# Performance work log

Hardware: AMD Instinct MI355X
Metric: run time of the kernel (lower is better)

The kernel has to match this reference:

```python
import jax, jax.numpy as jnp
import numpy as np

B, K, C, O, I = 32, 1024, 64, 32, 32  # batch, num_capsules, num_classes, out_dim, in_dim
NUM_ROUTING = 3


def squash(x, axis=-1):
    sq = jnp.sum(x * x, axis=axis, keepdims=True)
    return (sq / (1.0 + sq)) * x / jnp.sqrt(sq + 1e-8)


def setup_inputs() -> dict:
    key = jax.random.key(0)
    kx, kw = jax.random.split(key)
    x = jax.random.normal(kx, (B, K, I), dtype=jnp.float32)
    W = jax.random.normal(kw, (K, C, O, I), dtype=jnp.float32) * 0.01
    return {"x": x, "W": W}


def reference(x, W):
    # u_hat[b,k,c,o] = sum_i W[k,c,o,i] * x[b,k,i]  (the torch repeat+matmul)
    u_hat = jnp.einsum('kcoi,bki->bkco', W, x)  # [B,K,C,O]
    b_ij = jnp.zeros((B, K, C, 1), dtype=x.dtype)
    c_ij = None
    v_j = None
    for i in range(NUM_ROUTING):
        c_ij = jax.nn.softmax(b_ij, axis=2)              # softmax over classes
        s_j = jnp.sum(c_ij * u_hat, axis=1, keepdims=True)  # [B,1,C,O]
        v_j = squash(s_j, axis=-1)
        if i < NUM_ROUTING - 1:
            agreement = jnp.sum(u_hat * v_j, axis=-1, keepdims=True)  # [B,K,C,1]
            b_ij = b_ij + agreement
    return v_j[:, 0], c_ij[..., 0]  # ([B,C,O], [B,K,C])
```

## Files before the change

kernel.cpp:

```cpp
#include <hip/hip_runtime.h>
#include <stdint.h>

#define Bb 32
#define Kk 1024
#define Cc 64
#define Oo 32
#define Ii 32

typedef __attribute__((ext_vector_type(8))) short bf16x8;
typedef __attribute__((ext_vector_type(4))) float f32x4;

__device__ __forceinline__ short f2bf(float f) {
    uint32_t u = __builtin_bit_cast(uint32_t, f);
    u += 0x7fffu + ((u >> 16) & 1u);
    return (short)(u >> 16);
}
__device__ __forceinline__ float bflo(uint32_t u) { return __builtin_bit_cast(float, u << 16); }
__device__ __forceinline__ float bfhi(uint32_t u) { return __builtin_bit_cast(float, u & 0xffff0000u); }
__device__ __forceinline__ uint32_t pk2(float a, float b) {
    return (uint32_t)(uint16_t)f2bf(a) | ((uint32_t)(uint16_t)f2bf(b) << 16);
}


__global__ __launch_bounds__(256) void k_uhat(const float* __restrict__ x,
                                              const float* __restrict__ W,
                                              uint32_t* __restrict__ uh) {
    const int k = blockIdx.x;
    const int lane = threadIdx.x & 63;
    const int wave = threadIdx.x >> 6;
    const int m = lane & 15;
    const int q = lane >> 4;

    bf16x8 bfrag[2];
#pragma unroll
    for (int nb = 0; nb < 2; ++nb) {
        const float* xp = x + (size_t)((nb * 16 + m) * Kk + k) * Ii + q * 8;
        f32x4 a = *(const f32x4*)xp;
        f32x4 b = *(const f32x4*)(xp + 4);
        bf16x8 t;
        t[0] = f2bf(a.x); t[1] = f2bf(a.y); t[2] = f2bf(a.z); t[3] = f2bf(a.w);
        t[4] = f2bf(b.x); t[5] = f2bf(b.y); t[6] = f2bf(b.z); t[7] = f2bf(b.w);
        bfrag[nb] = t;
    }

    for (int cc = 0; cc < 16; ++cc) {
        const int c = wave * 16 + cc;
        bf16x8 afrag[2];
#pragma unroll
        for (int mo = 0; mo < 2; ++mo) {
            const float* wp = W + (size_t)((k * Cc + c) * Oo + mo * 16 + m) * Ii + q * 8;
            f32x4 a = __builtin_nontemporal_load((const f32x4*)wp);
            f32x4 b = __builtin_nontemporal_load((const f32x4*)(wp + 4));
            bf16x8 t;
            t[0] = f2bf(a.x); t[1] = f2bf(a.y); t[2] = f2bf(a.z); t[3] = f2bf(a.w);
            t[4] = f2bf(b.x); t[5] = f2bf(b.y); t[6] = f2bf(b.z); t[7] = f2bf(b.w);
            afrag[mo] = t;
        }
        const f32x4 z = {0.f, 0.f, 0.f, 0.f};
        f32x4 d0 = __builtin_amdgcn_mfma_f32_16x16x32_bf16(afrag[0], bfrag[0], z, 0, 0, 0);
        f32x4 d1 = __builtin_amdgcn_mfma_f32_16x16x32_bf16(afrag[0], bfrag[1], z, 0, 0, 0);
        f32x4 d2 = __builtin_amdgcn_mfma_f32_16x16x32_bf16(afrag[1], bfrag[0], z, 0, 0, 0);
        f32x4 d3 = __builtin_amdgcn_mfma_f32_16x16x32_bf16(afrag[1], bfrag[1], z, 0, 0, 0);

        uint4 p0, p1;
        p0.x = pk2(d0.x, d0.y); p0.y = pk2(d0.z, d0.w);
        p0.z = pk2(d1.x, d1.y); p0.w = pk2(d1.z, d1.w);
        p1.x = pk2(d2.x, d2.y); p1.y = pk2(d2.z, d2.w);
        p1.z = pk2(d3.x, d3.y); p1.w = pk2(d3.z, d3.w);
        uint32_t* dst = uh + (size_t)(k * Cc + c) * 512 + lane * 4;
        *(uint4*)dst = p0;
        *(uint4*)(dst + 256) = p1;
    }
}

__global__ __launch_bounds__(256) void k_sacc0(const uint32_t* __restrict__ uh,
                                               float* __restrict__ part0) {
    const int lane = threadIdx.x & 63;
    const int wave = threadIdx.x >> 6;
    const int c = (blockIdx.x & 15) * 4 + wave;
    const int chunk = blockIdx.x >> 4;
    const int k0 = chunk * 32;

    float acc[16];
#pragma unroll
    for (int i = 0; i < 16; ++i) acc[i] = 0.f;

    for (int kl = 0; kl < 32; ++kl) {
        const uint32_t* up = uh + (size_t)((k0 + kl) * Cc + c) * 512 + lane * 4;
        uint4 q0 = *(const uint4*)up;
        uint4 q1 = *(const uint4*)(up + 256);
        const float w0 = 1.0f / 64.0f;
        acc[0]  += w0 * bflo(q0.x);  acc[1]  += w0 * bfhi(q0.x);
        acc[2]  += w0 * bflo(q0.y);  acc[3]  += w0 * bfhi(q0.y);
        acc[4]  += w0 * bflo(q0.z);  acc[5]  += w0 * bfhi(q0.z);
        acc[6]  += w0 * bflo(q0.w);  acc[7]  += w0 * bfhi(q0.w);
        acc[8]  += w0 * bflo(q1.x);  acc[9]  += w0 * bfhi(q1.x);
        acc[10] += w0 * bflo(q1.y);  acc[11] += w0 * bfhi(q1.y);
        acc[12] += w0 * bflo(q1.z);  acc[13] += w0 * bfhi(q1.z);
        acc[14] += w0 * bflo(q1.w);  acc[15] += w0 * bfhi(q1.w);
    }
#pragma unroll
    for (int t = 0; t < 4; ++t) {
        f32x4 v = {acc[t * 4 + 0], acc[t * 4 + 1], acc[t * 4 + 2], acc[t * 4 + 3]};
        *(f32x4*)&part0[(((size_t)(chunk * Cc + c) * 4 + t) * 64 + lane) * 4] = v;
    }
}

__global__ __launch_bounds__(256) void k_reduce0(const float* __restrict__ part0,
                                                 float* __restrict__ vfrag) {
    __shared__ float red[4 * 64 * 17];
    const int c = blockIdx.x;
    const int tid = threadIdx.x;
    const int lane = tid & 63;
    const int cg = tid >> 6;

    float acc[16];
#pragma unroll
    for (int i = 0; i < 16; ++i) acc[i] = 0.f;
    for (int ch = cg * 8; ch < cg * 8 + 8; ++ch) {
        const f32x4* p = (const f32x4*)part0 + (size_t)(ch * Cc + c) * 4 * 64 + lane;
#pragma unroll
        for (int t = 0; t < 4; ++t) {
            f32x4 v = p[t * 64];
            acc[t * 4 + 0] += v.x; acc[t * 4 + 1] += v.y;
            acc[t * 4 + 2] += v.z; acc[t * 4 + 3] += v.w;
        }
    }
#pragma unroll
    for (int i = 0; i < 16; ++i) red[(cg * 64 + lane) * 17 + i] = acc[i];
    __syncthreads();

    if (tid < 64) {
        float a[16];
#pragma unroll
        for (int i = 0; i < 16; ++i)
            a[i] = red[tid * 17 + i] + red[(64 + tid) * 17 + i]
                 + red[(128 + tid) * 17 + i] + red[(192 + tid) * 17 + i];
        float sq0 = 0.f, sq1 = 0.f;
#pragma unroll
        for (int r = 0; r < 4; ++r) {
            sq0 += a[r] * a[r] + a[8 + r] * a[8 + r];
            sq1 += a[4 + r] * a[4 + r] + a[12 + r] * a[12 + r];
        }
        sq0 += __shfl_xor(sq0, 16); sq0 += __shfl_xor(sq0, 32);
        sq1 += __shfl_xor(sq1, 16); sq1 += __shfl_xor(sq1, 32);
        const float c0 = sq0 / ((1.f + sq0) * sqrtf(sq0 + 1e-8f));
        const float c1 = sq1 / ((1.f + sq1) * sqrtf(sq1 + 1e-8f));
#pragma unroll
        for (int r = 0; r < 4; ++r) {
            a[r] *= c0; a[8 + r] *= c0;
            a[4 + r] *= c1; a[12 + r] *= c1;
        }
        float* vp = vfrag + ((size_t)c * 64 + tid) * 16;
#pragma unroll
        for (int t = 0; t < 4; ++t) {
            f32x4 v = {a[t * 4 + 0], a[t * 4 + 1], a[t * 4 + 2], a[t * 4 + 3]};
            *(f32x4*)(vp + t * 4) = v;
        }
    }
}

template <bool FINAL>
__global__ __launch_bounds__(512) void k_iter(const uint32_t* __restrict__ uh,
                                              const float* __restrict__ vfrag,
                                              float* __restrict__ bbuf,
                                              uint32_t* __restrict__ partB,
                                              float* __restrict__ outc) {
    __shared__ float agr[4 * 64 * 32];
    const int tid = threadIdx.x;
    const int lane = tid & 63;
    const int w = tid >> 6;
    const int m = lane & 15;
    const int q = lane >> 4;
    const int k0 = blockIdx.x * 4;

    for (int cc = 0; cc < 8; ++cc) {
        const int c = w * 8 + cc;
        const float* vp = vfrag + ((size_t)c * 64 + lane) * 16;
        f32x4 vv0 = *(const f32x4*)(vp);
        f32x4 vv1 = *(const f32x4*)(vp + 4);
        f32x4 vv2 = *(const f32x4*)(vp + 8);
        f32x4 vv3 = *(const f32x4*)(vp + 12);
#pragma unroll
        for (int kl = 0; kl < 4; ++kl) {
            const uint32_t* up = uh + (size_t)((k0 + kl) * Cc + c) * 512 + lane * 4;
            uint4 q0 = *(const uint4*)up;
            uint4 q1 = *(const uint4*)(up + 256);
            float p0 = bflo(q0.x) * vv0.x + bfhi(q0.x) * vv0.y
                     + bflo(q0.y) * vv0.z + bfhi(q0.y) * vv0.w
                     + bflo(q1.x) * vv2.x + bfhi(q1.x) * vv2.y
                     + bflo(q1.y) * vv2.z + bfhi(q1.y) * vv2.w;
            float p1 = bflo(q0.z) * vv1.x + bfhi(q0.z) * vv1.y
                     + bflo(q0.w) * vv1.z + bfhi(q0.w) * vv1.w
                     + bflo(q1.z) * vv3.x + bfhi(q1.z) * vv3.y
                     + bflo(q1.w) * vv3.z + bfhi(q1.w) * vv3.w;
            p0 += __shfl_xor(p0, 16);
            p0 += __shfl_xor(p0, 32);
            p1 += __shfl_xor(p1, 16);
            p1 += __shfl_xor(p1, 32);
            if (q == 0) {
                agr[(kl * 64 + c) * 32 + m] = p0;
                agr[(kl * 64 + c) * 32 + 16 + m] = p1;
            }
        }
    }
    __syncthreads();

    if (tid < 128) {
        const int kl = tid >> 5;
        const int b = tid & 31;
        const int k = k0 + kl;
        float row[64];
#pragma unroll
        for (int c = 0; c < 64; ++c) row[c] = agr[(kl * 64 + c) * 32 + b];
        if (!FINAL) {
            float* bp = bbuf + (size_t)(k * Bb + b) * Cc;
#pragma unroll
            for (int c = 0; c < 64; ++c) bp[c] = row[c];
        } else {
            const float* bp = bbuf + (size_t)(k * Bb + b) * Cc;
#pragma unroll
            for (int c = 0; c < 64; ++c) row[c] += bp[c];
        }
        float mx = row[0];
#pragma unroll
        for (int c = 1; c < 64; ++c) mx = fmaxf(mx, row[c]);
        float sum = 0.f;
#pragma unroll
        for (int c = 0; c < 64; ++c) { row[c] = __expf(row[c] - mx); sum += row[c]; }
        const float inv = 1.f / sum;
#pragma unroll
        for (int c = 0; c < 64; ++c) row[c] *= inv;
        if (FINAL) {
            float* op = outc + (size_t)(b * Kk + k) * Cc;
#pragma unroll
            for (int c = 0; c < 64; ++c) op[c] = row[c];
        }
#pragma unroll
        for (int c = 0; c < 64; ++c) agr[(kl * 64 + c) * 32 + b] = row[c];
    }
    __syncthreads();

    const int chunk = blockIdx.x;
    for (int cg = 0; cg < 8; ++cg) {
        const int c = w * 8 + cg;
        float acc[16];
#pragma unroll
        for (int i = 0; i < 16; ++i) acc[i] = 0.f;
#pragma unroll
        for (int kl = 0; kl < 4; ++kl) {
            const uint32_t* up = uh + (size_t)((k0 + kl) * Cc + c) * 512 + lane * 4;
            uint4 q0 = *(const uint4*)up;
            uint4 q1 = *(const uint4*)(up + 256);
            const float w0 = agr[(kl * 64 + c) * 32 + m];
            const float w1 = agr[(kl * 64 + c) * 32 + 16 + m];
            acc[0]  += w0 * bflo(q0.x);  acc[1]  += w0 * bfhi(q0.x);
            acc[2]  += w0 * bflo(q0.y);  acc[3]  += w0 * bfhi(q0.y);
            acc[4]  += w1 * bflo(q0.z);  acc[5]  += w1 * bfhi(q0.z);
            acc[6]  += w1 * bflo(q0.w);  acc[7]  += w1 * bfhi(q0.w);
            acc[8]  += w0 * bflo(q1.x);  acc[9]  += w0 * bfhi(q1.x);
            acc[10] += w0 * bflo(q1.y);  acc[11] += w0 * bfhi(q1.y);
            acc[12] += w1 * bflo(q1.z);  acc[13] += w1 * bfhi(q1.z);
            acc[14] += w1 * bflo(q1.w);  acc[15] += w1 * bfhi(q1.w);
        }
        uint4 o0, o1;
        o0.x = pk2(acc[0],  acc[1]);  o0.y = pk2(acc[2],  acc[3]);
        o0.z = pk2(acc[4],  acc[5]);  o0.w = pk2(acc[6],  acc[7]);
        o1.x = pk2(acc[8],  acc[9]);  o1.y = pk2(acc[10], acc[11]);
        o1.z = pk2(acc[12], acc[13]); o1.w = pk2(acc[14], acc[15]);
        uint32_t* dst = partB + ((size_t)(c * 256 + chunk) * 64 + lane) * 8;
        *(uint4*)dst = o0;
        *(uint4*)(dst + 4) = o1;
    }
}

__global__ __launch_bounds__(256) void k_red1(const uint32_t* __restrict__ partB,
                                              float* __restrict__ part2) {
    __shared__ float red[4 * 64 * 17];
    const int cb = blockIdx.x;
    const int c = cb >> 3;
    const int g = cb & 7;
    const int tid = threadIdx.x;
    const int lane = tid & 63;
    const int ww = tid >> 6;

    float acc[16];
#pragma unroll
    for (int i = 0; i < 16; ++i) acc[i] = 0.f;
    for (int ch = g * 32 + ww * 8; ch < g * 32 + ww * 8 + 8; ++ch) {
        const uint32_t* p = partB + ((size_t)(c * 256 + ch) * 64 + lane) * 8;
        uint4 a = *(const uint4*)p;
        uint4 b = *(const uint4*)(p + 4);
        acc[0]  += bflo(a.x);  acc[1]  += bfhi(a.x);
        acc[2]  += bflo(a.y);  acc[3]  += bfhi(a.y);
        acc[4]  += bflo(a.z);  acc[5]  += bfhi(a.z);
        acc[6]  += bflo(a.w);  acc[7]  += bfhi(a.w);
        acc[8]  += bflo(b.x);  acc[9]  += bfhi(b.x);
        acc[10] += bflo(b.y);  acc[11] += bfhi(b.y);
        acc[12] += bflo(b.z);  acc[13] += bfhi(b.z);
        acc[14] += bflo(b.w);  acc[15] += bfhi(b.w);
    }
#pragma unroll
    for (int i = 0; i < 16; ++i) red[(ww * 64 + lane) * 17 + i] = acc[i];
    __syncthreads();

    if (tid < 64) {
        float a[16];
#pragma unroll
        for (int i = 0; i < 16; ++i)
            a[i] = red[tid * 17 + i] + red[(64 + tid) * 17 + i]
                 + red[(128 + tid) * 17 + i] + red[(192 + tid) * 17 + i];
        float* dst = part2 + ((size_t)cb * 64 + tid) * 16;
#pragma unroll
        for (int t = 0; t < 4; ++t) {
            f32x4 v = {a[t * 4 + 0], a[t * 4 + 1], a[t * 4 + 2], a[t * 4 + 3]};
            *(f32x4*)(dst + t * 4) = v;
        }
    }
}

template <bool FINAL>
__global__ __launch_bounds__(64) void k_red2(const float* __restrict__ part2,
                                             float* __restrict__ vfrag,
                                             float* __restrict__ out_v) {
    const int c = blockIdx.x;
    const int lane = threadIdx.x;
    const int m = lane & 15;
    const int q = lane >> 4;

    float a[16];
#pragma unroll
    for (int i = 0; i < 16; ++i) a[i] = 0.f;
    for (int g = 0; g < 8; ++g) {
        const float* p = part2 + ((size_t)(c * 8 + g) * 64 + lane) * 16;
#pragma unroll
        for (int t = 0; t < 4; ++t) {
            f32x4 v = *(const f32x4*)(p + t * 4);
            a[t * 4 + 0] += v.x; a[t * 4 + 1] += v.y;
            a[t * 4 + 2] += v.z; a[t * 4 + 3] += v.w;
        }
    }
    float sq0 = 0.f, sq1 = 0.f;
#pragma unroll
    for (int r = 0; r < 4; ++r) {
        sq0 += a[r] * a[r] + a[8 + r] * a[8 + r];
        sq1 += a[4 + r] * a[4 + r] + a[12 + r] * a[12 + r];
    }
    sq0 += __shfl_xor(sq0, 16); sq0 += __shfl_xor(sq0, 32);
    sq1 += __shfl_xor(sq1, 16); sq1 += __shfl_xor(sq1, 32);
    const float c0 = sq0 / ((1.f + sq0) * sqrtf(sq0 + 1e-8f));
    const float c1 = sq1 / ((1.f + sq1) * sqrtf(sq1 + 1e-8f));
#pragma unroll
    for (int r = 0; r < 4; ++r) {
        a[r] *= c0; a[8 + r] *= c0;
        a[4 + r] *= c1; a[12 + r] *= c1;
    }
    float* vp = vfrag + ((size_t)c * 64 + lane) * 16;
#pragma unroll
    for (int t = 0; t < 4; ++t) {
        f32x4 v = {a[t * 4 + 0], a[t * 4 + 1], a[t * 4 + 2], a[t * 4 + 3]};
        *(f32x4*)(vp + t * 4) = v;
    }
    if (FINAL) {
#pragma unroll
        for (int t = 0; t < 4; ++t)
#pragma unroll
            for (int r = 0; r < 4; ++r) {
                const int b = (t & 1) * 16 + m;
                const int o = (t >> 1) * 16 + q * 4 + r;
                out_v[((size_t)b * Cc + c) * Oo + o] = a[t * 4 + r];
            }
    }
}

extern "C" void kernel_launch(void* const* d_in, const int* in_sizes, int n_in,
                              void* d_out, int out_size, void* d_ws, size_t ws_size,
                              hipStream_t stream) {
    (void)in_sizes; (void)n_in; (void)out_size;
    const float* x = (const float*)d_in[0];
    const float* W = (const float*)d_in[1];
    float* out_v = (float*)d_out;
    float* out_c = out_v + Bb * Cc * Oo;

    char* ws = (char*)d_ws;
    const size_t UH_BYTES = (size_t)Kk * Cc * 512 * 4;
    const size_t P0_BYTES = (size_t)32 * Cc * 4 * 64 * 4 * 4;
    const size_t PB_BYTES = (size_t)Cc * 256 * 64 * 8 * 4;
    const size_t P2_BYTES = (size_t)512 * 64 * 16 * 4;
    const size_t BB_BYTES = (size_t)Kk * Bb * Cc * 4;
    const size_t VF_BYTES = (size_t)Cc * 64 * 16 * 4;

    uint32_t* uh = (uint32_t*)ws;                      ws += UH_BYTES;
    float* part0  = (float*)ws;                        ws += P0_BYTES;
    uint32_t* partB = (uint32_t*)ws;                   ws += PB_BYTES;
    float* part2  = (float*)ws;                        ws += P2_BYTES;
    float* bbuf   = (float*)ws;                        ws += BB_BYTES;
    float* vfrag  = (float*)ws;                        ws += VF_BYTES;
    const size_t NEED = UH_BYTES + P0_BYTES + PB_BYTES + P2_BYTES + BB_BYTES + VF_BYTES;
    if (ws_size < NEED) return;

    k_uhat<<<Kk, 256, 0, stream>>>(x, W, uh);
    k_sacc0<<<512, 256, 0, stream>>>(uh, part0);
    k_reduce0<<<Cc, 256, 0, stream>>>(part0, vfrag);
    k_iter<false><<<256, 512, 0, stream>>>(uh, vfrag, bbuf, partB, nullptr);
    k_red1<<<512, 256, 0, stream>>>(partB, part2);
    k_red2<false><<<Cc, 64, 0, stream>>>(part2, vfrag, nullptr);
    k_iter<true><<<256, 512, 0, stream>>>(uh, vfrag, bbuf, partB, out_c);
    k_red1<<<512, 256, 0, stream>>>(partB, part2);
    k_red2<true><<<Cc, 64, 0, stream>>>(part2, vfrag, out_v);
}
```

Measured before the change: 526.0 us.

## Fuse first routing sum into u_hat GEMM and pre-pack x as bf16

The first routing pass's uniform-weighted sum over capsules is now accumulated inside the u_hat MFMA kernel, so the separate pass that re-read the whole bf16 u_hat buffer is gone. Blocks are reorganised to own a chunk of capsules for one group of classes, and x is pre-converted to a packed bf16 layout by a small new kernel so MFMA B fragments load directly. The partial buffer grows and the 1/64 scaling moves into the reduction. The sum now uses fp32 MFMA results instead of rounded bf16 values, which changes numerics slightly.

Result: faster. 507.8 us (-3.5%).

```diff
diff --git a/kernel.cpp b/kernel.cpp
--- a/kernel.cpp
+++ b/kernel.cpp
@@ -22,45 +22,60 @@
 }
 
 
-__global__ __launch_bounds__(256) void k_uhat(const float* __restrict__ x,
+__global__ __launch_bounds__(256) void k_xT(const float* __restrict__ x,
+                                            uint32_t* __restrict__ xT) {
+    const int k = blockIdx.x;
+    const int tid = threadIdx.x;
+    const int b = tid >> 3;
+    const int i8 = (tid & 7) * 4;
+    const float* xp = x + ((size_t)b * Kk + k) * Ii + i8;
+    f32x4 v = *(const f32x4*)xp;
+    uint32_t* dst = xT + (size_t)k * 512 + b * 16 + i8 / 2;
+    dst[0] = pk2(v.x, v.y);
+    dst[1] = pk2(v.z, v.w);
+}
+
+__global__ __launch_bounds__(256) void k_uhat(const uint32_t* __restrict__ xT,
                                               const float* __restrict__ W,
-                                              uint32_t* __restrict__ uh) {
-    const int k = blockIdx.x;
+                                              uint32_t* __restrict__ uh,
+                                              float* __restrict__ part0) {
+    const int kchunk = blockIdx.x & 63;
+    const int cgroup = blockIdx.x >> 6;
     const int lane = threadIdx.x & 63;
     const int wave = threadIdx.x >> 6;
+    const int c = cgroup * 4 + wave;
     const int m = lane & 15;
     const int q = lane >> 4;
 
-    bf16x8 bfrag[2];
-#pragma unroll
-    for (int nb = 0; nb < 2; ++nb) {
-        const float* xp = x + (size_t)((nb * 16 + m) * Kk + k) * Ii + q * 8;
-        f32x4 a = *(const f32x4*)xp;
-        f32x4 b = *(const f32x4*)(xp + 4);
-        bf16x8 t;
-        t[0] = f2bf(a.x); t[1] = f2bf(a.y); t[2] = f2bf(a.z); t[3] = f2bf(a.w);
-        t[4] = f2bf(b.x); t[5] = f2bf(b.y); t[6] = f2bf(b.z); t[7] = f2bf(b.w);
-        bfrag[nb] = t;
-    }
-
-    for (int cc = 0; cc < 16; ++cc) {
-        const int c = wave * 16 + cc;
-        bf16x8 afrag[2];
-#pragma unroll
-        for (int mo = 0; mo < 2; ++mo) {
-            const float* wp = W + (size_t)((k * Cc + c) * Oo + mo * 16 + m) * Ii + q * 8;
-            f32x4 a = __builtin_nontemporal_load((const f32x4*)wp);
-            f32x4 b = __builtin_nontemporal_load((const f32x4*)(wp + 4));
+    float acc[16];
+#pragma unroll
+    for (int i = 0; i < 16; ++i) acc[i] = 0.f;
+
+    for (int kl = 0; kl < 16; ++kl) {
+        const int k = kchunk * 16 + kl;
+        const uint32_t* xp = xT + (size_t)k * 512 + m * 16 + q * 4;
+        bf16x8 b0 = *(const bf16x8*)xp;
+        bf16x8 b1 = *(const bf16x8*)(xp + 256);
+        bf16x8 a0, a1;
+        {
+            const float* wp = W + (size_t)((k * Cc + c) * Oo + m) * Ii + q * 8;
+            f32x4 u0 = __builtin_nontemporal_load((const f32x4*)wp);
+            f32x4 u1 = __builtin_nontemporal_load((const f32x4*)(wp + 4));
+            f32x4 u2 = __builtin_nontemporal_load((const f32x4*)(wp + 512));
+            f32x4 u3 = __builtin_nontemporal_load((const f32x4*)(wp + 516));
             bf16x8 t;
-            t[0] = f2bf(a.x); t[1] = f2bf(a.y); t[2] = f2bf(a.z); t[3] = f2bf(a.w);
-            t[4] = f2bf(b.x); t[5] = f2bf(b.y); t[6] = f2bf(b.z); t[7] = f2bf(b.w);
-            afrag[mo] = t;
+            t[0] = f2bf(u0.x); t[1] = f2bf(u0.y); t[2] = f2bf(u0.z); t[3] = f2bf(u0.w);
+            t[4] = f2bf(u1.x); t[5] = f2bf(u1.y); t[6] = f2bf(u1.z); t[7] = f2bf(u1.w);
+            a0 = t;
+            t[0] = f2bf(u2.x); t[1] = f2bf(u2.y); t[2] = f2bf(u2.z); t[3] = f2bf(u2.w);
+            t[4] = f2bf(u3.x); t[5] = f2bf(u3.y); t[6] = f2bf(u3.z); t[7] = f2bf(u3.w);
+            a1 = t;
         }
         const f32x4 z = {0.f, 0.f, 0.f, 0.f};
-        f32x4 d0 = __builtin_amdgcn_mfma_f32_16x16x32_bf16(afrag[0], bfrag[0], z, 0, 0, 0);
-        f32x4 d1 = __builtin_amdgcn_mfma_f32_16x16x32_bf16(afrag[0], bfrag[1], z, 0, 0, 0);
-        f32x4 d2 = __builtin_amdgcn_mfma_f32_16x16x32_bf16(afrag[1], bfrag[0], z, 0, 0, 0);
-        f32x4 d3 = __builtin_amdgcn_mfma_f32_16x16x32_bf16(afrag[1], bfrag[1], z, 0, 0, 0);
+        f32x4 d0 = __builtin_amdgcn_mfma_f32_16x16x32_bf16(a0, b0, z, 0, 0, 0);
+        f32x4 d1 = __builtin_amdgcn_mfma_f32_16x16x32_bf16(a0, b1, z, 0, 0, 0);
+        f32x4 d2 = __builtin_amdgcn_mfma_f32_16x16x32_bf16(a1, b0, z, 0, 0, 0);
+        f32x4 d3 = __builtin_amdgcn_mfma_f32_16x16x32_bf16(a1, b1, z, 0, 0, 0);
 
         uint4 p0, p1;
         p0.x = pk2(d0.x, d0.y); p0.y = pk2(d0.z, d0.w);
@@ -70,72 +85,49 @@
         uint32_t* dst = uh + (size_t)(k * Cc + c) * 512 + lane * 4;
         *(uint4*)dst = p0;
         *(uint4*)(dst + 256) = p1;
-    }
-}
-
-__global__ __launch_bounds__(256) void k_sacc0(const uint32_t* __restrict__ uh,
-                                               float* __restrict__ part0) {
-    const int lane = threadIdx.x & 63;
-    const int wave = threadIdx.x >> 6;
-    const int c = (blockIdx.x & 15) * 4 + wave;
-    const int chunk = blockIdx.x >> 4;
-    const int k0 = chunk * 32;
-
-    float acc[16];
-#pragma unroll
-    for (int i = 0; i < 16; ++i) acc[i] = 0.f;
-
-    for (int kl = 0; kl < 32; ++kl) {
-        const uint32_t* up = uh + (size_t)((k0 + kl) * Cc + c) * 512 + lane * 4;
-        uint4 q0 = *(const uint4*)up;
-        uint4 q1 = *(const uint4*)(up + 256);
-        const float w0 = 1.0f / 64.0f;
-        acc[0]  += w0 * bflo(q0.x);  acc[1]  += w0 * bfhi(q0.x);
-        acc[2]  += w0 * bflo(q0.y);  acc[3]  += w0 * bfhi(q0.y);
-        acc[4]  += w0 * bflo(q0.z);  acc[5]  += w0 * bfhi(q0.z);
-        acc[6]  += w0 * bflo(q0.w);  acc[7]  += w0 * bfhi(q0.w);
-        acc[8]  += w0 * bflo(q1.x);  acc[9]  += w0 * bfhi(q1.x);
-        acc[10] += w0 * bflo(q1.y);  acc[11] += w0 * bfhi(q1.y);
-        acc[12] += w0 * bflo(q1.z);  acc[13] += w0 * bfhi(q1.z);
-        acc[14] += w0 * bflo(q1.w);  acc[15] += w0 * bfhi(q1.w);
+
+        acc[0]  += d0.x; acc[1]  += d0.y; acc[2]  += d0.z; acc[3]  += d0.w;
+        acc[4]  += d1.x; acc[5]  += d1.y; acc[6]  += d1.z; acc[7]  += d1.w;
+        acc[8]  += d2.x; acc[9]  += d2.y; acc[10] += d2.z; acc[11] += d2.w;
+        acc[12] += d3.x; acc[13] += d3.y; acc[14] += d3.z; acc[15] += d3.w;
     }
 #pragma unroll
     for (int t = 0; t < 4; ++t) {
         f32x4 v = {acc[t * 4 + 0], acc[t * 4 + 1], acc[t * 4 + 2], acc[t * 4 + 3]};
-        *(f32x4*)&part0[(((size_t)(chunk * Cc + c) * 4 + t) * 64 + lane) * 4] = v;
-    }
-}
-
-__global__ __launch_bounds__(256) void k_reduce0(const float* __restrict__ part0,
-                                                 float* __restrict__ vfrag) {
+        *(f32x4*)&part0[(((size_t)(kchunk * Cc + c)) * 64 + lane) * 16 + t * 4] = v;
+    }
+}
+
+__global__ __launch_bounds__(256) void k_redA(const float* __restrict__ part0,
+                                              float* __restrict__ vfrag) {
     __shared__ float red[4 * 64 * 17];
     const int c = blockIdx.x;
     const int tid = threadIdx.x;
     const int lane = tid & 63;
-    const int cg = tid >> 6;
+    const int grp = tid >> 6;
 
     float acc[16];
 #pragma unroll
     for (int i = 0; i < 16; ++i) acc[i] = 0.f;
-    for (int ch = cg * 8; ch < cg * 8 + 8; ++ch) {
-        const f32x4* p = (const f32x4*)part0 + (size_t)(ch * Cc + c) * 4 * 64 + lane;
+    for (int ch = grp * 16; ch < grp * 16 + 16; ++ch) {
+        const float* p = part0 + (((size_t)(ch * Cc + c)) * 64 + lane) * 16;
 #pragma unroll
         for (int t = 0; t < 4; ++t) {
-            f32x4 v = p[t * 64];
+            f32x4 v = *(const f32x4*)(p + t * 4);
             acc[t * 4 + 0] += v.x; acc[t * 4 + 1] += v.y;
             acc[t * 4 + 2] += v.z; acc[t * 4 + 3] += v.w;
         }
     }
 #pragma unroll
-    for (int i = 0; i < 16; ++i) red[(cg * 64 + lane) * 17 + i] = acc[i];
+    for (int i = 0; i < 16; ++i) red[(grp * 64 + lane) * 17 + i] = acc[i];
     __syncthreads();
 
     if (tid < 64) {
         float a[16];
 #pragma unroll
         for (int i = 0; i < 16; ++i)
-            a[i] = red[tid * 17 + i] + red[(64 + tid) * 17 + i]
-                 + red[(128 + tid) * 17 + i] + red[(192 + tid) * 17 + i];
+            a[i] = (red[tid * 17 + i] + red[(64 + tid) * 17 + i]
+                  + red[(128 + tid) * 17 + i] + red[(192 + tid) * 17 + i]) * (1.f / 64.f);
         float sq0 = 0.f, sq1 = 0.f;
 #pragma unroll
         for (int r = 0; r < 4; ++r) {
@@ -384,24 +376,26 @@
 
     char* ws = (char*)d_ws;
     const size_t UH_BYTES = (size_t)Kk * Cc * 512 * 4;
-    const size_t P0_BYTES = (size_t)32 * Cc * 4 * 64 * 4 * 4;
+    const size_t XT_BYTES = (size_t)Kk * 512 * 4;
+    const size_t P0_BYTES = (size_t)64 * Cc * 64 * 16 * 4;
     const size_t PB_BYTES = (size_t)Cc * 256 * 64 * 8 * 4;
     const size_t P2_BYTES = (size_t)512 * 64 * 16 * 4;
     const size_t BB_BYTES = (size_t)Kk * Bb * Cc * 4;
     const size_t VF_BYTES = (size_t)Cc * 64 * 16 * 4;
 
     uint32_t* uh = (uint32_t*)ws;                      ws += UH_BYTES;
+    uint32_t* xT = (uint32_t*)ws;                      ws += XT_BYTES;
     float* part0  = (float*)ws;                        ws += P0_BYTES;
     uint32_t* partB = (uint32_t*)ws;                   ws += PB_BYTES;
     float* part2  = (float*)ws;                        ws += P2_BYTES;
     float* bbuf   = (float*)ws;                        ws += BB_BYTES;
     float* vfrag  = (float*)ws;                        ws += VF_BYTES;
-    const size_t NEED = UH_BYTES + P0_BYTES + PB_BYTES + P2_BYTES + BB_BYTES + VF_BYTES;
+    const size_t NEED = UH_BYTES + XT_BYTES + P0_BYTES + PB_BYTES + P2_BYTES + BB_BYTES + VF_BYTES;
     if (ws_size < NEED) return;
 
-    k_uhat<<<Kk, 256, 0, stream>>>(x, W, uh);
-    k_sacc0<<<512, 256, 0, stream>>>(uh, part0);
-    k_reduce0<<<Cc, 256, 0, stream>>>(part0, vfrag);
+    k_xT<<<Kk, 256, 0, stream>>>(x, xT);
+    k_uhat<<<1024, 256, 0, stream>>>(xT, W, uh, part0);
+    k_redA<<<Cc, 256, 0, stream>>>(part0, vfrag);
     k_iter<false><<<256, 512, 0, stream>>>(uh, vfrag, bbuf, partB, nullptr);
     k_red1<<<512, 256, 0, stream>>>(partB, part2);
     k_red2<false><<<Cc, 64, 0, stream>>>(part2, vfrag, nullptr);
```
